# Performance work log

Measured on AMD Instinct MI355X. Metric: run time of the kernel, lower is better.

Reference implementation:

```python
import jax, jax.numpy as jnp
import numpy as np

B, S, H = 8, 8192, 512

def setup_inputs() -> dict:
    key = jax.random.key(0)
    k1, k2, k3, k4 = jax.random.split(key, 4)
    hidden = jax.random.normal(k1, (1, B, H), dtype=jnp.float32)
    encoder_outputs = jax.random.normal(k2, (B, S, H), dtype=jnp.float32)
    W = jax.random.normal(k3, (H, H), dtype=jnp.float32) * (1.0 / np.sqrt(H))
    b = jax.random.normal(k4, (H,), dtype=jnp.float32) * 0.01
    return {"hidden": hidden, "encoder_outputs": encoder_outputs, "W": W, "b": b}

def reference(hidden, encoder_outputs, W, b):
    # method='general': energy_k = Linear(enc[:,k]) ; score_k = bmm(energy_k[:,None,:], hidden.permute(1,2,0)).sum()
    # hidden: [1,B,H] -> h: [B,H]
    h = hidden[0]
    proj = jnp.einsum('bsh,kh->bsk', encoder_outputs, W) + b  # Linear: x @ W.T + b -> [B,S,H]
    attn_energies = jnp.einsum('bsh,bh->bs', proj, h)         # [B,S]
    return jax.nn.softmax(attn_energies, axis=1)
```

## Files before the change

### kernel.cpp

```cpp
#include <hip/hip_runtime.h>
#include <math.h>

#define Hd 512
#define Bn 8
#define Sn 8192

__global__ __launch_bounds__(256) void k_proj(const float* __restrict__ hidden,
                                              const float* __restrict__ W,
                                              float* __restrict__ v) {
    const int b  = blockIdx.x;
    const int kc = blockIdx.y;
    const int t  = threadIdx.x;
    __shared__ float hs[32];
    if (t < 32) hs[t] = hidden[b * Hd + kc * 32 + t];
    __syncthreads();
    float acc0 = 0.f, acc1 = 0.f;
    const float* Wp = W + (size_t)(kc * 32) * Hd;
    #pragma unroll
    for (int k = 0; k < 32; ++k) {
        const float hk = hs[k];
        acc0 += hk * Wp[(size_t)k * Hd + t];
        acc1 += hk * Wp[(size_t)k * Hd + t + 256];
    }
    atomicAdd(&v[b * Hd + t],       acc0);
    atomicAdd(&v[b * Hd + t + 256], acc1);
}

__global__ __launch_bounds__(256) void k_energy(const float* __restrict__ enc,
                                                const float* __restrict__ v,
                                                float* __restrict__ e) {
    const int b    = blockIdx.y;
    const int wave = threadIdx.x >> 6;
    const int lane = threadIdx.x & 63;

    const float4* vp = (const float4*)(v + b * Hd);
    const float4 v0 = vp[lane];
    const float4 v1 = vp[64 + lane];

    const int row0 = blockIdx.x * 64 + wave * 16;
    const float4* base = (const float4*)(enc + ((size_t)b * Sn + row0) * Hd);

    #pragma unroll 4
    for (int r = 0; r < 16; ++r) {
        const float4* rowp = base + (size_t)r * (Hd / 4);
        const float4 a0 = rowp[lane];
        const float4 a1 = rowp[64 + lane];
        float p = a0.x * v0.x + a0.y * v0.y + a0.z * v0.z + a0.w * v0.w
                + a1.x * v1.x + a1.y * v1.y + a1.z * v1.z + a1.w * v1.w;
        #pragma unroll
        for (int off = 32; off >= 1; off >>= 1)
            p += __shfl_xor(p, off, 64);
        if (lane == 0) e[(size_t)b * Sn + row0 + r] = p;
    }
}

__global__ __launch_bounds__(1024) void k_softmax(const float* __restrict__ e,
                                                  float* __restrict__ out) {
    const int b = blockIdx.x;
    const int t = threadIdx.x;
    const int wave = t >> 6, lane = t & 63;
    const float* eb = e + (size_t)b * Sn;

    float vals[8];
    float m = -INFINITY;
    #pragma unroll
    for (int i = 0; i < 8; ++i) {
        vals[i] = eb[t + i * 1024];
        m = fmaxf(m, vals[i]);
    }
    #pragma unroll
    for (int off = 32; off >= 1; off >>= 1)
        m = fmaxf(m, __shfl_xor(m, off, 64));

    __shared__ float red[16];
    if (lane == 0) red[wave] = m;
    __syncthreads();
    if (t < 16) {
        float mm = red[t];
        #pragma unroll
        for (int off = 8; off >= 1; off >>= 1)
            mm = fmaxf(mm, __shfl_xor(mm, off, 16));
        if (t == 0) red[0] = mm;
    }
    __syncthreads();
    m = red[0];
    __syncthreads();

    float s = 0.f;
    #pragma unroll
    for (int i = 0; i < 8; ++i) {
        vals[i] = __expf(vals[i] - m);
        s += vals[i];
    }
    #pragma unroll
    for (int off = 32; off >= 1; off >>= 1)
        s += __shfl_xor(s, off, 64);
    if (lane == 0) red[wave] = s;
    __syncthreads();
    if (t < 16) {
        float ss = red[t];
        #pragma unroll
        for (int off = 8; off >= 1; off >>= 1)
            ss += __shfl_xor(ss, off, 16);
        if (t == 0) red[0] = ss;
    }
    __syncthreads();
    const float inv = 1.0f / red[0];

    #pragma unroll
    for (int i = 0; i < 8; ++i)
        out[(size_t)b * Sn + t + i * 1024] = vals[i] * inv;
}

extern "C" void kernel_launch(void* const* d_in, const int* in_sizes, int n_in,
                              void* d_out, int out_size, void* d_ws, size_t ws_size,
                              hipStream_t stream) {
    const float* hidden = (const float*)d_in[0];
    const float* enc    = (const float*)d_in[1];
    const float* W      = (const float*)d_in[2];
    float* out = (float*)d_out;

    float* v = (float*)d_ws;
    float* e = v + Bn * Hd;

    hipMemsetAsync(v, 0, Bn * Hd * sizeof(float), stream);
    k_proj   <<<dim3(Bn, 16),     256,  0, stream>>>(hidden, W, v);
    k_energy <<<dim3(Sn / 64, Bn), 256, 0, stream>>>(enc, v, e);
    k_softmax<<<Bn,               1024, 0, stream>>>(e, out);
}
```

Measured before the change: 37.65 us.

## Replace atomic projection reduction with partial buffers summed in energy kernel

The projection kernel now writes per-chunk partial vectors instead of atomically accumulating, which removes the memset launch and the atomics. The energy kernel sums the 16 partials itself and processes 8 rows per wave instead of 16, doubling the grid. It also batches four row reductions with a transposed shuffle pattern to cut shuffle count. Each energy block now rereads 16 partial vectors (32KB per b), adding redundant L2 traffic in exchange for fewer launches.

After: 35.38 us. 1.06x faster.

```diff
diff --git a/kernel.cpp b/kernel.cpp
--- a/kernel.cpp
+++ b/kernel.cpp
@@ -4,10 +4,11 @@
 #define Hd 512
 #define Bn 8
 #define Sn 8192
+#define KC 16
 
 __global__ __launch_bounds__(256) void k_proj(const float* __restrict__ hidden,
                                               const float* __restrict__ W,
-                                              float* __restrict__ v) {
+                                              float* __restrict__ vpart) {
     const int b  = blockIdx.x;
     const int kc = blockIdx.y;
     const int t  = threadIdx.x;
@@ -22,35 +23,57 @@
         acc0 += hk * Wp[(size_t)k * Hd + t];
         acc1 += hk * Wp[(size_t)k * Hd + t + 256];
     }
-    atomicAdd(&v[b * Hd + t],       acc0);
-    atomicAdd(&v[b * Hd + t + 256], acc1);
+    float* vo = vpart + ((size_t)kc * Bn + b) * Hd;
+    vo[t]       = acc0;
+    vo[t + 256] = acc1;
 }
 
 __global__ __launch_bounds__(256) void k_energy(const float* __restrict__ enc,
-                                                const float* __restrict__ v,
+                                                const float* __restrict__ vpart,
                                                 float* __restrict__ e) {
     const int b    = blockIdx.y;
     const int wave = threadIdx.x >> 6;
     const int lane = threadIdx.x & 63;
 
-    const float4* vp = (const float4*)(v + b * Hd);
-    const float4 v0 = vp[lane];
-    const float4 v1 = vp[64 + lane];
+    float4 v0 = make_float4(0.f, 0.f, 0.f, 0.f);
+    float4 v1 = make_float4(0.f, 0.f, 0.f, 0.f);
+    #pragma unroll 4
+    for (int kc = 0; kc < KC; ++kc) {
+        const float4* sp = (const float4*)(vpart + ((size_t)kc * Bn + b) * Hd);
+        const float4 a = sp[lane];
+        const float4 c = sp[64 + lane];
+        v0.x += a.x; v0.y += a.y; v0.z += a.z; v0.w += a.w;
+        v1.x += c.x; v1.y += c.y; v1.z += c.z; v1.w += c.w;
+    }
 
-    const int row0 = blockIdx.x * 64 + wave * 16;
+    const int row0 = blockIdx.x * 32 + wave * 8;
     const float4* base = (const float4*)(enc + ((size_t)b * Sn + row0) * Hd);
 
-    #pragma unroll 4
-    for (int r = 0; r < 16; ++r) {
-        const float4* rowp = base + (size_t)r * (Hd / 4);
-        const float4 a0 = rowp[lane];
-        const float4 a1 = rowp[64 + lane];
-        float p = a0.x * v0.x + a0.y * v0.y + a0.z * v0.z + a0.w * v0.w
-                + a1.x * v1.x + a1.y * v1.y + a1.z * v1.z + a1.w * v1.w;
+    #pragma unroll
+    for (int rb = 0; rb < 8; rb += 4) {
+        float p[4];
         #pragma unroll
-        for (int off = 32; off >= 1; off >>= 1)
-            p += __shfl_xor(p, off, 64);
-        if (lane == 0) e[(size_t)b * Sn + row0 + r] = p;
+        for (int r = 0; r < 4; ++r) {
+            const float4* rowp = base + (size_t)(rb + r) * (Hd / 4);
+            const float4 a0 = rowp[lane];
+            const float4 a1 = rowp[64 + lane];
+            p[r] = a0.x * v0.x + a0.y * v0.y + a0.z * v0.z + a0.w * v0.w
+                 + a1.x * v1.x + a1.y * v1.y + a1.z * v1.z + a1.w * v1.w;
+        }
+        float s0 = p[0] + __shfl_xor(p[0], 1, 64);
+        float s1 = p[1] + __shfl_xor(p[1], 1, 64);
+        float s2 = p[2] + __shfl_xor(p[2], 1, 64);
+        float s3 = p[3] + __shfl_xor(p[3], 1, 64);
+        float t0 = (lane & 1) ? s1 : s0;
+        float t1 = (lane & 1) ? s3 : s2;
+        t0 += __shfl_xor(t0, 2, 64);
+        t1 += __shfl_xor(t1, 2, 64);
+        float w = (lane & 2) ? t1 : t0;
+        w += __shfl_xor(w, 4, 64);
+        w += __shfl_xor(w, 8, 64);
+        w += __shfl_xor(w, 16, 64);
+        w += __shfl_xor(w, 32, 64);
+        if (lane < 4) e[(size_t)b * Sn + row0 + rb + lane] = w;
     }
 }
 
@@ -120,11 +143,10 @@
     const float* W      = (const float*)d_in[2];
     float* out = (float*)d_out;
 
-    float* v = (float*)d_ws;
-    float* e = v + Bn * Hd;
+    float* vpart = (float*)d_ws;
+    float* e     = vpart + KC * Bn * Hd;
 
-    hipMemsetAsync(v, 0, Bn * Hd * sizeof(float), stream);
-    k_proj   <<<dim3(Bn, 16),     256,  0, stream>>>(hidden, W, v);
-    k_energy <<<dim3(Sn / 64, Bn), 256, 0, stream>>>(enc, v, e);
-    k_softmax<<<Bn,               1024, 0, stream>>>(e, out);
+    k_proj   <<<dim3(Bn, KC),      256,  0, stream>>>(hidden, W, vpart);
+    k_energy <<<dim3(Sn / 32, Bn), 256,  0, stream>>>(enc, vpart, e);
+    k_softmax<<<Bn,                1024, 0, stream>>>(e, out);
 }
```
